# Kernel optimization log

Hardware: AMD Instinct MI355X
Metric: run time of the kernel (lower is better)

Reference implementation:

```python
import jax, jax.numpy as jnp
import numpy as np
from jax import lax

B, N, D = 4, 64, 32  # graphs, nodes/graph, volume side
HC = 1024            # hidden_channels
NF = 2048            # num_node_features = 32*(D//8)**3
NC = 4               # num_classes
LC = 256             # linear_channels = N*(HC//4)//64


def setup_inputs() -> dict:
    key = jax.random.key(0)
    ks = jax.random.split(key, 16)
    x = jax.random.normal(ks[0], (B, N, D, D, D), jnp.float32)
    # binary symmetric adjacency, zero diagonal (edge presence only; GCNConv ignores values)
    u = jax.random.uniform(ks[1], (B, N, N))
    a = (u < 0.2).astype(jnp.int32)
    a = jnp.maximum(a, a.transpose(0, 2, 1)) * (1 - jnp.eye(N, dtype=jnp.int32))
    s = 0.05
    inp = dict(
        x=x, adj=a, batch_size=B,
        w_conv1=jax.random.normal(ks[2], (16, 1, 3, 3, 3), jnp.float32) * s,
        b_conv1=jnp.zeros((16,), jnp.float32),
        w_conv2=jax.random.normal(ks[3], (32, 16, 3, 3, 3), jnp.float32) * s,
        b_conv2=jnp.zeros((32,), jnp.float32),
        w_g1=jax.random.normal(ks[4], (NF, HC), jnp.float32) * s,
        b_g1=jnp.zeros((HC,), jnp.float32),
        w_g2=jax.random.normal(ks[5], (HC, HC // 2), jnp.float32) * s,
        b_g2=jnp.zeros((HC // 2,), jnp.float32),
        w_g3=jax.random.normal(ks[6], (HC // 2, HC // 4), jnp.float32) * s,
        b_g3=jnp.zeros((HC // 4,), jnp.float32),
        w_fc1=jax.random.normal(ks[7], (LC, 2 * LC), jnp.float32) * s,
        b_fc1=jnp.zeros((2 * LC,), jnp.float32),
        w_fc2=jax.random.normal(ks[8], (2 * LC, NC), jnp.float32) * s,
        b_fc2=jnp.zeros((NC,), jnp.float32),
    )
    return inp


DN = ('NCDHW', 'OIDHW', 'NCDHW')


def _maxpool3(h):
    # MaxPool3d(kernel=3, stride=2, padding=1); pad value -inf matches torch
    return lax.reduce_window(h, -jnp.inf, lax.max,
                             (1, 1, 3, 3, 3), (1, 1, 2, 2, 2),
                             [(0, 0), (0, 0), (1, 1), (1, 1), (1, 1)])


def _gcn_norm(adj, dtype):
    # GCNConv: A_hat = A + I, sym-normalized D^-1/2 A_hat D^-1/2 (per graph)
    A = (adj != 0).astype(dtype) + jnp.eye(adj.shape[-1], dtype=dtype)[None]
    deg = A.sum(-1)                        # [B, N], >= 1
    dinv = deg ** -0.5
    return A * dinv[:, :, None] * dinv[:, None, :]


def _forward(x, adj, batch_size, w_conv1, b_conv1, w_conv2, b_conv2,
             w_g1, b_g1, w_g2, b_g2, w_g3, b_g3, w_fc1, b_fc1, w_fc2, b_fc2):
    b, n = x.shape[0], x.shape[1]
    v = x.reshape(b * n, 1, x.shape[2], x.shape[3], x.shape[4])
    h = lax.conv_general_dilated(v, w_conv1, (1, 1, 1), [(1, 1)] * 3, dimension_numbers=DN)
    h = jax.nn.relu(h + b_conv1[None, :, None, None, None])
    h = _maxpool3(h)                                     # [BN,16,16,16,16]
    h = lax.conv_general_dilated(h, w_conv2, (2, 2, 2), [(1, 1)] * 3, dimension_numbers=DN)
    h = jax.nn.relu(h + b_conv2[None, :, None, None, None])
    h = _maxpool3(h)                                     # [BN,32,4,4,4]
    feat = h.reshape(b, n, -1)                           # [B,N,2048]

    A_norm = _gcn_norm(adj, feat.dtype)                  # [B,N,N]
    gcn = lambda X, W, bb: jnp.einsum('bij,bjf->bif', A_norm, X @ W) + bb
    g = jax.nn.relu(gcn(feat, w_g1, b_g1))
    g = jax.nn.relu(gcn(g, w_g2, b_g2))
    g = gcn(g, w_g3, b_g3)                               # [B,N,256] (no relu, matches source)

    g = g.reshape(batch_size, -1)                        # [B, 16384]
    g = g.reshape(batch_size, -1, 64).max(-1)            # MaxPool1d(64) on 2D input -> [B,256]
    g = jax.nn.relu(g @ w_fc1 + b_fc1)
    return jax.nn.softmax(g @ w_fc2 + b_fc2, axis=-1)


def reference(x, adj, batch_size, w_conv1, b_conv1, w_conv2, b_conv2,
              w_g1, b_g1, w_g2, b_g2, w_g3, b_g3, w_fc1, b_fc1, w_fc2, b_fc2):
    return _forward(x, adj, batch_size, w_conv1, b_conv1, w_conv2, b_conv2,
                    w_g1, b_g1, w_g2, b_g2, w_g3, b_g3, w_fc1, b_fc1, w_fc2, b_fc2)
```

## Files before the change

### kernel.cpp

```cpp
#include <hip/hip_runtime.h>

typedef unsigned short ushort_t;
typedef unsigned long long ull_t;
typedef __attribute__((ext_vector_type(8))) short bf16x8;
typedef __attribute__((ext_vector_type(4))) float f32x4;

static __device__ __forceinline__ unsigned short f2bf(float f) {
  unsigned u = __float_as_uint(f);
  u = (u + 0x7FFFu + ((u >> 16) & 1u)) >> 16;
  return (unsigned short)u;
}

static __device__ __forceinline__ f32x4 max4(f32x4 a, f32x4 b) {
  f32x4 r;
  r[0] = fmaxf(a[0], b[0]); r[1] = fmaxf(a[1], b[1]);
  r[2] = fmaxf(a[2], b[2]); r[3] = fmaxf(a[3], b[3]);
  return r;
}

static __device__ __forceinline__ void gbar(int* bar0, int bid, bool do_wait) {
  __syncthreads();
  if (threadIdx.x == 0) {
    int* bar = bar0 + (bid << 10);
    __threadfence();
    const int leaf = (blockIdx.x & 7) << 5;
    if (__hip_atomic_fetch_add(&bar[leaf], 1, __ATOMIC_ACQ_REL,
                               __HIP_MEMORY_SCOPE_AGENT) == 7) {
      if (__hip_atomic_fetch_add(&bar[256], 1, __ATOMIC_ACQ_REL,
                                 __HIP_MEMORY_SCOPE_AGENT) == 7) {
#pragma unroll
        for (int i = 0; i < 8; ++i)
          __hip_atomic_store(&bar[288 + (i << 5)], 1, __ATOMIC_RELEASE,
                             __HIP_MEMORY_SCOPE_AGENT);
      }
    }
    if (do_wait) {
      int* mygen = &bar[288 + leaf];
      for (int it = 0; it < (1 << 22); ++it) {
        if (__hip_atomic_load(mygen, __ATOMIC_RELAXED,
                              __HIP_MEMORY_SCOPE_AGENT) != 0) break;
        __builtin_amdgcn_s_sleep(2);
      }
      __threadfence();
    }
  }
  __syncthreads();
}


__device__ __forceinline__ void prep_transpose(
    const float* __restrict__ W, ushort_t* __restrict__ out,
    int K, int N, int n0, int k0, int t, float (*tile)[33])
{
  const int tx = t & 31, ty = t >> 5;
#pragma unroll
  for (int i = 0; i < 4; ++i) {
    const int k = k0 + ty + i * 8;
    tile[ty + i * 8][tx] = W[(size_t)k * N + n0 + tx];
  }
  __syncthreads();
#pragma unroll
  for (int i = 0; i < 4; ++i) {
    const int n = n0 + ty + i * 8;
    out[(size_t)n * K + k0 + tx] = f2bf(tile[tx][ty + i * 8]);
  }
}

__global__ __launch_bounds__(256) void k_prep(
    const float* __restrict__ x, ushort_t* __restrict__ xb16,
    const float* __restrict__ w2, ushort_t* __restrict__ w2f,
    const float* __restrict__ wg1, ushort_t* __restrict__ wg1T,
    const float* __restrict__ wg2, ushort_t* __restrict__ wg2T,
    const float* __restrict__ wg3, ushort_t* __restrict__ wg3T,
    const int* __restrict__ adj, float* __restrict__ An)
{
  __shared__ float tile[32][33];
  __shared__ float dinv[64];
  __shared__ int part[256];
  int b = blockIdx.x;
  const int t = threadIdx.x;
  if (b < 8192) {
    const int tid = b * 256 + t;
    const float4 v = ((const float4*)x)[tid];
    const unsigned lo = (unsigned)f2bf(v.x) | ((unsigned)f2bf(v.y) << 16);
    const unsigned hi = (unsigned)f2bf(v.z) | ((unsigned)f2bf(v.w) << 16);
    ((uint2*)xb16)[tid] = make_uint2(lo, hi);
    return;
  }
  b -= 8192;
  if (b < 56) {
    const int tid = b * 256 + t;
    if (tid < 14336) {
      const int nt = tid / 7168, rem = tid % 7168;
      const int kk = rem / 512, rem2 = rem % 512;
      const int l = rem2 >> 3, j = rem2 & 7;
      const int n = nt * 16 + (l & 15);
      const int k = (l >> 4) * 8 + kk * 32 + j;
      float v = 0.f;
      if (k < 432) v = w2[n * 432 + k];
      w2f[tid] = f2bf(v);
    }
    return;
  }
  b -= 56;
  if (b < 2048) { prep_transpose(wg1, wg1T, 2048, 1024, (b & 31) << 5, (b >> 5) << 5, t, tile); return; }
  b -= 2048;
  if (b < 512)  { prep_transpose(wg2, wg2T, 1024, 512,  (b & 15) << 5, (b >> 4) << 5, t, tile); return; }
  b -= 512;
  if (b < 128)  { prep_transpose(wg3, wg3T, 512,  256,  (b & 7)  << 5, (b >> 3) << 5, t, tile); return; }
  b -= 128;
  {
    const int i = t >> 2, q = t & 3;
    const int* ab = adj + b * 4096 + i * 64 + q * 16;
    int d = 0;
#pragma unroll
    for (int j = 0; j < 16; ++j) d += (ab[j] != 0) ? 1 : 0;
    part[t] = d;
    __syncthreads();
    if (q == 0)
      dinv[i] = rsqrtf((float)(1 + part[t] + part[t + 1] + part[t + 2] + part[t + 3]));
    __syncthreads();
    for (int idx = t; idx < 4096; idx += 256) {
      const int ii = idx >> 6, jj = idx & 63;
      const float a = (ii == jj) ? 1.f : ((adj[b * 4096 + idx] != 0) ? 1.f : 0.f);
      An[b * 4096 + idx] = a * dinv[ii] * dinv[jj];
    }
  }
}

__global__ __launch_bounds__(256) void k_conv1_mfma(
    const ushort_t* __restrict__ xb16, const float* __restrict__ wc,
    const float* __restrict__ bc, ushort_t* __restrict__ h1)
{
  __shared__ ushort_t L[2 * 34 * 76];
  char* Lb = (char*)L;
  const int bn = blockIdx.x >> 3, zg = blockIdx.x & 7;
  const int t = threadIdx.x;
  const int w = t >> 6, l = t & 63;
  const int grp = l >> 4, m = l & 15, ch = l & 15;
  const float NINF = -1e30f;

  union { short s[8]; bf16x8 v; } uA, uB;
#pragma unroll
  for (int j = 0; j < 8; ++j) {
    const int k = grp * 8 + j;
    float wA = 0.f, wB = 0.f;
    if (k < 12) {
      const int dx = k >> 2, dz = k & 3;
      if (dz < 3) { wA = wc[ch*27 + dz*9 + 0 + dx]; wB = wc[ch*27 + dz*9 + 6 + dx]; }
    } else if (k >= 16 && k < 28) {
      const int kk = k - 16, dx = kk >> 2, dz = kk & 3;
      if (dz < 3) wA = wc[ch*27 + dz*9 + 3 + dx];
    }
    uA.s[j] = (short)f2bf(wA);
    uB.s[j] = (short)f2bf(wB);
  }

  int aX1[3], aX2[3];
#pragma unroll
  for (int s = 0; s < 3; ++s) {
    const int Q1 = 2*m + s + 2*(grp & 1);
    const int Q2 = Q1 + 1;
    aX1[s] = (Q1 & 1) * 5168 + (Q1 >> 1) * 8;
    aX2[s] = (Q2 & 1) * 5168 + (Q2 >> 1) * 8;
  }
  const int rsel = (grp >> 1) * 152;

  for (int u = t; u < 200; u += 256) {
    int addr;
    if (u < 72) {
      const int rr = (u < 36) ? 0 : 33;
      const int s = (u < 36) ? u : u - 36;
      const int pp = s / 18, slot = s - pp * 18;
      addr = pp * 5168 + rr * 152 + slot * 8;
    } else {
      const int v = u - 72;
      const int rr = 1 + (v >> 2);
      const int pp = (v >> 1) & 1;
      const int slot = (v & 1) * 17;
      addr = pp * 5168 + rr * 152 + slot * 8;
    }
    *(ull_t*)(Lb + addr) = 0ull;
  }

  f32x4 accZ[4][2];
#pragma unroll
  for (int j = 0; j < 4; ++j)
#pragma unroll
    for (int p = 0; p < 2; ++p) accZ[j][p] = (f32x4){NINF, NINF, NINF, NINF};

  const ushort_t* xb = xb16 + (size_t)bn * 32768;

#pragma unroll 1
  for (int ci = 0; ci < 5; ++ci) {
    const int cz = 4*zg - 1 + ci;
    if (cz < 0) continue;
    if (t < 128) {
      const int r = 1 + (t >> 2), g = t & 3;
      const ushort_t* xrow = xb + (r - 1) * 32 + g * 8;
      uint4 u0 = make_uint4(0u, 0u, 0u, 0u), u2 = make_uint4(0u, 0u, 0u, 0u);
      if (cz > 0)  u0 = *(const uint4*)(xrow + (cz - 1) * 1024);
      const uint4 u1 = *(const uint4*)(xrow + cz * 1024);
      if (cz < 31) u2 = *(const uint4*)(xrow + (cz + 1) * 1024);
      char* b0 = Lb + r * 152 + (4 * g + 1) * 8;
      char* b1 = Lb + 5168 + r * 152 + (4 * g + 1) * 8;
      const unsigned* p0 = (const unsigned*)&u0;
      const unsigned* p1 = (const unsigned*)&u1;
      const unsigned* p2 = (const unsigned*)&u2;
#pragma unroll
      for (int e = 0; e < 4; ++e) {
        const unsigned w0 = p0[e], w1 = p1[e], w2v = p2[e];
        const unsigned lo_e = (w0 & 0xFFFFu) | (w1 << 16);
        const unsigned hi_e = (w2v & 0xFFFFu);
        const unsigned lo_o = (w0 >> 16) | (w1 & 0xFFFF0000u);
        const unsigned hi_o = (w2v >> 16);
        *(ull_t*)(b0 + e * 8) = (ull_t)lo_e | ((ull_t)hi_e << 32);
        *(ull_t*)(b1 + e * 8) = (ull_t)lo_o | ((ull_t)hi_o << 32);
      }
    }
    __syncthreads();
    f32x4 accP0 = (f32x4){NINF, NINF, NINF, NINF};
    f32x4 accP1 = (f32x4){NINF, NINF, NINF, NINF};
#pragma unroll
    for (int yy = 0; yy < 9; ++yy) {
      if (yy == 0 && w == 0) continue;
      const int y = 8 * w - 1 + yy;
      const int rbA = y * 152 + rsel;
      const int rbB = (y + 2) * 152;
      f32x4 Cy;
#pragma unroll
      for (int s = 0; s < 3; ++s) {
        union { ull_t u[2]; bf16x8 v; } fA, fB;
        fA.u[0] = *(const ull_t*)(Lb + aX1[s] + rbA);
        fA.u[1] = *(const ull_t*)(Lb + aX2[s] + rbA);
        fB.u[0] = *(const ull_t*)(Lb + aX1[s] + rbB);
        fB.u[1] = *(const ull_t*)(Lb + aX2[s] + rbB);
        f32x4 acc = (f32x4){0.f, 0.f, 0.f, 0.f};
        acc = __builtin_amdgcn_mfma_f32_16x16x32_bf16(fA.v, uA.v, acc, 0, 0, 0);
        acc = __builtin_amdgcn_mfma_f32_16x16x32_bf16(fB.v, uB.v, acc, 0, 0, 0);
        if (s == 0) acc[0] = (l < 16) ? NINF : acc[0];
        Cy = (s == 0) ? acc : max4(Cy, acc);
      }
      if (yy & 1) {
        const int c = (yy - 1) / 2;
        if ((c & 1) == 0) accP0 = max4(accP0, Cy); else accP1 = max4(accP1, Cy);
      } else {
        const int cl = yy / 2 - 1;
        const int chh = yy / 2;
        if (cl >= 0) {
          if ((cl & 1) == 0) {
            accP0 = max4(accP0, Cy);
            if (ci <= 2) accZ[cl][0] = max4(accZ[cl][0], accP0);
            if (ci >= 2) accZ[cl][1] = max4(accZ[cl][1], accP0);
            accP0 = (f32x4){NINF, NINF, NINF, NINF};
          } else {
            accP1 = max4(accP1, Cy);
            if (ci <= 2) accZ[cl][0] = max4(accZ[cl][0], accP1);
            if (ci >= 2) accZ[cl][1] = max4(accZ[cl][1], accP1);
            accP1 = (f32x4){NINF, NINF, NINF, NINF};
          }
        }
        if (chh <= 3) {
          if ((chh & 1) == 0) accP0 = max4(accP0, Cy); else accP1 = max4(accP1, Cy);
        }
      }
    }
    __syncthreads();
  }

  const float biasv = bc[ch];
#pragma unroll
  for (int j = 0; j < 4; ++j) {
    const int py = 4 * w + j;
#pragma unroll
    for (int p = 0; p < 2; ++p) {
      const int pz = 2 * zg + p;
      const f32x4 v = accZ[j][p];
      const unsigned lo = (unsigned)f2bf(fmaxf(v[0] + biasv, 0.f)) |
                          ((unsigned)f2bf(fmaxf(v[1] + biasv, 0.f)) << 16);
      const unsigned hi = (unsigned)f2bf(fmaxf(v[2] + biasv, 0.f)) |
                          ((unsigned)f2bf(fmaxf(v[3] + biasv, 0.f)) << 16);
      ushort_t* dst = h1 + (((size_t)(bn * 16 + ch) * 16 + pz) << 8) + py * 16 + grp * 4;
      *(uint2*)dst = make_uint2(lo, hi);
    }
  }
}

__global__ __launch_bounds__(128) void k_conv2(
    const ushort_t* __restrict__ h1, const ushort_t* __restrict__ w2f,
    float* __restrict__ c2)
{
  __shared__ ushort_t U[16 * 456];
  ushort_t* Hs = U;
  unsigned* Hsd = (unsigned*)U;
  ushort_t* As = U;
  const int b = blockIdx.x;
  const int bn = b >> 5, oz = (b >> 2) & 7, yg = b & 3;
  const int t = threadIdx.x;
  const ushort_t* hb = h1 + ((size_t)bn << 16);
  const int w = t >> 6, l = t & 63;

  bf16x8 bfr[14];
#pragma unroll
  for (int kk = 0; kk < 14; ++kk)
    bfr[kk] = *(const bf16x8*)(const void*)&w2f[(((w * 14) + kk) * 64 + l) * 8];

#pragma unroll
  for (int it = 0; it < 9; ++it) {
    const int u = t + it * 128;
    const int row = u >> 2, q = u & 3;
    const int ic = row / 18;
    const int r2 = row - ic * 18;
    const int izp = r2 / 6;
    const int iyp = r2 - izp * 6;
    const int iz = 2 * oz - 1 + izp;
    const int iy = 4 * yg - 1 + iyp;
    uint2 v = make_uint2(0u, 0u);
    if ((unsigned)iz < 16u && (unsigned)iy < 16u)
      v = *(const uint2*)(hb + (ic << 12) + (iz << 8) + (iy << 4) + q * 4);
    *(uint2*)&Hs[row * 20 + q * 4] = v;
  }
  __syncthreads();

  const int m = t >> 3, sub = t & 7;
  const int ox = m & 7;
  const int my = (m >> 3) * 2;
  ushort_t tv[54];
  int j = 0;
#pragma unroll
  for (int ic2 = 0; ic2 < 2; ++ic2) {
    const int ic = sub * 2 + ic2;
#pragma unroll
    for (int dz = 0; dz < 3; ++dz) {
#pragma unroll
      for (int dy = 0; dy < 3; ++dy) {
        const int row = ic * 18 + dz * 6 + my + dy;
        const unsigned* rp = Hsd + row * 10;
        const unsigned d0 = (ox > 0) ? rp[ox - 1] : 0u;
        const unsigned d1 = rp[ox];
        tv[j]     = (ushort_t)(d0 >> 16);
        tv[j + 1] = (ushort_t)(d1 & 0xFFFFu);
        tv[j + 2] = (ushort_t)(d1 >> 16);
        j += 3;
      }
    }
  }
  __syncthreads();

  {
    unsigned* Aw = (unsigned*)As;
    const int wbase = m * 228 + sub * 27;
#pragma unroll
    for (int p = 0; p < 27; ++p)
      Aw[wbase + p] = (unsigned)tv[2 * p] | ((unsigned)tv[2 * p + 1] << 16);
    Aw[(t >> 3) * 228 + 216 + (t & 7)] = 0u;
  }
  __syncthreads();

  f32x4 acc = {0.f, 0.f, 0.f, 0.f};
  const ushort_t* arow = &As[(l & 15) * 456 + ((l >> 4) << 3)];
#pragma unroll
  for (int kk = 0; kk < 14; ++kk) {
    const bf16x8 af = *(const bf16x8*)(const void*)&arow[kk * 32];
    acc = __builtin_amdgcn_mfma_f32_16x16x32_bf16(af, bfr[kk], acc, 0, 0, 0);
  }
  const int n = w * 16 + (l & 15);
  const int m0 = (l >> 4) << 2;
  float* cb = c2 + (((size_t)(bn * 32 + n) * 8) + oz) * 64 + yg * 16 + m0;
  *(float4*)cb = make_float4(acc[0], acc[1], acc[2], acc[3]);
}

__global__ __launch_bounds__(256) void k_pool2(
    const float* __restrict__ c2, const float* __restrict__ bc2,
    ushort_t* __restrict__ featb, int* __restrict__ bar)
{
  if (blockIdx.x == 0) {
    for (int i = threadIdx.x; i < 4096; i += 256) bar[i] = 0;
  }
  const int tid = blockIdx.x * 256 + threadIdx.x;
  const int bn = tid >> 9, r = tid & 511;
  const int ch = r >> 4, pz = (r >> 2) & 3, py = r & 3;
  const float* base = c2 + ((size_t)(bn * 32 + ch) << 9);
  float m0 = -1e30f, m1 = -1e30f, m2 = -1e30f, m3 = -1e30f;
#pragma unroll
  for (int dz = 0; dz < 3; ++dz) {
    const int oz = 2 * pz - 1 + dz;
    if ((unsigned)oz >= 8u) continue;
#pragma unroll
    for (int dy = 0; dy < 3; ++dy) {
      const int oy = 2 * py - 1 + dy;
      if ((unsigned)oy >= 8u) continue;
      const float* row = base + (oz << 6) + (oy << 3);
      const float4 a = ((const float4*)row)[0];
      const float4 b = ((const float4*)row)[1];
      m0 = fmaxf(m0, fmaxf(a.x, a.y));
      m1 = fmaxf(m1, fmaxf(a.y, fmaxf(a.z, a.w)));
      m2 = fmaxf(m2, fmaxf(a.w, fmaxf(b.x, b.y)));
      m3 = fmaxf(m3, fmaxf(b.y, fmaxf(b.z, b.w)));
    }
  }
  const float bb = bc2[ch];
  const unsigned lo = (unsigned)f2bf(fmaxf(m0 + bb, 0.f)) |
                      ((unsigned)f2bf(fmaxf(m1 + bb, 0.f)) << 16);
  const unsigned hi = (unsigned)f2bf(fmaxf(m2 + bb, 0.f)) |
                      ((unsigned)f2bf(fmaxf(m3 + bb, 0.f)) << 16);
  *(uint2*)(featb + (size_t)bn * 2048 + r * 4) = make_uint2(lo, hi);
}

__device__ __forceinline__ void gcn_body(
    const ushort_t* __restrict__ Xb, const ushort_t* __restrict__ WT,
    const float* __restrict__ bias, const float* __restrict__ An,
    ushort_t* __restrict__ Ob, float* __restrict__ spw,
    int K, int N, int relu, int b, int jb,
    ushort_t (*As)[64 * 72], ushort_t (*Bs)[64 * 72], ushort_t* Ps)
{
  const int t = threadIdx.x, w = t >> 6, l = t & 63;
  const int r0 = t >> 3, kc0 = t & 7;
  const int lm = l & 15, lg = l >> 4;

  union { short s[8]; bf16x8 v; } afr[2];
  {
    const float* ap = An + b * 4096 + (16 * w + lm) * 64 + (lg << 3);
#pragma unroll
    for (int kc = 0; kc < 2; ++kc) {
      const float4 v0 = *(const float4*)(ap + kc * 32);
      const float4 v1 = *(const float4*)(ap + kc * 32 + 4);
      afr[kc].s[0] = (short)f2bf(v0.x); afr[kc].s[1] = (short)f2bf(v0.y);
      afr[kc].s[2] = (short)f2bf(v0.z); afr[kc].s[3] = (short)f2bf(v0.w);
      afr[kc].s[4] = (short)f2bf(v1.x); afr[kc].s[5] = (short)f2bf(v1.y);
      afr[kc].s[6] = (short)f2bf(v1.z); afr[kc].s[7] = (short)f2bf(v1.w);
    }
  }

  f32x4 acc[4];
#pragma unroll
  for (int nt = 0; nt < 4; ++nt) acc[nt] = (f32x4){0.f, 0.f, 0.f, 0.f};

  const ushort_t* arow0 = &Xb[(size_t)(b * 64 + r0) * K + kc0 * 8];
  const ushort_t* arow1 = &Xb[(size_t)(b * 64 + r0 + 32) * K + kc0 * 8];
  const ushort_t* brow0 = &WT[(size_t)(jb + r0) * K + kc0 * 8];
  const ushort_t* brow1 = &WT[(size_t)(jb + r0 + 32) * K + kc0 * 8];

  uint4 vaA0 = *(const uint4*)arow0;
  uint4 vaA1 = *(const uint4*)arow1;
  uint4 vbA0 = *(const uint4*)brow0;
  uint4 vbA1 = *(const uint4*)brow1;
  uint4 vaB0 = *(const uint4*)(arow0 + 64);
  uint4 vaB1 = *(const uint4*)(arow1 + 64);
  uint4 vbB0 = *(const uint4*)(brow0 + 64);
  uint4 vbB1 = *(const uint4*)(brow1 + 64);

  int buf = 0;
#pragma unroll 1
  for (int kt = 0; kt < K; kt += 128) {
    *(uint4*)&As[buf][r0 * 72 + kc0 * 8]        = vaA0;
    *(uint4*)&As[buf][(r0 + 32) * 72 + kc0 * 8] = vaA1;
    *(uint4*)&Bs[buf][r0 * 72 + kc0 * 8]        = vbA0;
    *(uint4*)&Bs[buf][(r0 + 32) * 72 + kc0 * 8] = vbA1;
    __syncthreads();
    if (kt + 128 < K) {
      vaA0 = *(const uint4*)(arow0 + kt + 128);
      vaA1 = *(const uint4*)(arow1 + kt + 128);
      vbA0 = *(const uint4*)(brow0 + kt + 128);
      vbA1 = *(const uint4*)(brow1 + kt + 128);
    }
#pragma unroll
    for (int ks = 0; ks < 2; ++ks) {
      const bf16x8 af = *(const bf16x8*)(const void*)
          &As[buf][(16 * w + lm) * 72 + ks * 32 + (lg << 3)];
#pragma unroll
      for (int nt = 0; nt < 4; ++nt) {
        const bf16x8 bf = *(const bf16x8*)(const void*)
            &Bs[buf][(nt * 16 + lm) * 72 + ks * 32 + (lg << 3)];
        acc[nt] = __builtin_amdgcn_mfma_f32_16x16x32_bf16(af, bf, acc[nt], 0, 0, 0);
      }
    }
    buf ^= 1;
    *(uint4*)&As[buf][r0 * 72 + kc0 * 8]        = vaB0;
    *(uint4*)&As[buf][(r0 + 32) * 72 + kc0 * 8] = vaB1;
    *(uint4*)&Bs[buf][r0 * 72 + kc0 * 8]        = vbB0;
    *(uint4*)&Bs[buf][(r0 + 32) * 72 + kc0 * 8] = vbB1;
    __syncthreads();
    if (kt + 192 < K) {
      vaB0 = *(const uint4*)(arow0 + kt + 192);
      vaB1 = *(const uint4*)(arow1 + kt + 192);
      vbB0 = *(const uint4*)(brow0 + kt + 192);
      vbB1 = *(const uint4*)(brow1 + kt + 192);
    }
#pragma unroll
    for (int ks = 0; ks < 2; ++ks) {
      const bf16x8 af = *(const bf16x8*)(const void*)
          &As[buf][(16 * w + lm) * 72 + ks * 32 + (lg << 3)];
#pragma unroll
      for (int nt = 0; nt < 4; ++nt) {
        const bf16x8 bf = *(const bf16x8*)(const void*)
            &Bs[buf][(nt * 16 + lm) * 72 + ks * 32 + (lg << 3)];
        acc[nt] = __builtin_amdgcn_mfma_f32_16x16x32_bf16(af, bf, acc[nt], 0, 0, 0);
      }
    }
    buf ^= 1;
  }

  __syncthreads();
  const int m0 = lg << 2;
#pragma unroll
  for (int nt = 0; nt < 4; ++nt) {
    const int n = nt * 16 + lm;
    const unsigned lo = (unsigned)f2bf(acc[nt][0]) | ((unsigned)f2bf(acc[nt][1]) << 16);
    const unsigned hi = (unsigned)f2bf(acc[nt][2]) | ((unsigned)f2bf(acc[nt][3]) << 16);
    *(uint2*)&Ps[n * 72 + 16 * w + m0] = make_uint2(lo, hi);
  }
  __syncthreads();

  float mx0 = -1e30f, mx1 = -1e30f, mx2 = -1e30f, mx3 = -1e30f;
#pragma unroll
  for (int nt = 0; nt < 4; ++nt) {
    const bf16x8 b0 = *(const bf16x8*)(const void*)&Ps[(nt * 16 + lm) * 72 + (lg << 3)];
    const bf16x8 b1 = *(const bf16x8*)(const void*)&Ps[(nt * 16 + lm) * 72 + 32 + (lg << 3)];
    f32x4 a2 = (f32x4){0.f, 0.f, 0.f, 0.f};
    a2 = __builtin_amdgcn_mfma_f32_16x16x32_bf16(afr[0].v, b0, a2, 0, 0, 0);
    a2 = __builtin_amdgcn_mfma_f32_16x16x32_bf16(afr[1].v, b1, a2, 0, 0, 0);
    const int col = jb + nt * 16 + lm;
    const float bv = bias[col];
    if (spw) {
      mx0 = fmaxf(mx0, a2[0] + bv);
      mx1 = fmaxf(mx1, a2[1] + bv);
      mx2 = fmaxf(mx2, a2[2] + bv);
      mx3 = fmaxf(mx3, a2[3] + bv);
    } else {
#pragma unroll
      for (int r = 0; r < 4; ++r) {
        const int row = b * 64 + 16 * w + m0 + r;
        float v = a2[r] + bv;
        if (relu) v = fmaxf(v, 0.f);
        Ob[(size_t)row * N + col] = f2bf(v);
      }
    }
  }
  if (spw) {
#pragma unroll
    for (int mk = 1; mk <= 8; mk <<= 1) {
      mx0 = fmaxf(mx0, __shfl_xor(mx0, mk));
      mx1 = fmaxf(mx1, __shfl_xor(mx1, mk));
      mx2 = fmaxf(mx2, __shfl_xor(mx2, mk));
      mx3 = fmaxf(mx3, __shfl_xor(mx3, mk));
    }
    if (lm == 0) {
      const int c = jb >> 6;
      const int n = 16 * w + m0;
      spw[b * 256 + (n + 0) * 4 + c] = mx0;
      spw[b * 256 + (n + 1) * 4 + c] = mx1;
      spw[b * 256 + (n + 2) * 4 + c] = mx2;
      spw[b * 256 + (n + 3) * 4 + c] = mx3;
    }
  }
}

__global__ __launch_bounds__(256) void k_tail(
    const ushort_t* __restrict__ featb,
    const ushort_t* __restrict__ wg1T, const float* __restrict__ bg1,
    const ushort_t* __restrict__ wg2T, const float* __restrict__ bg2,
    const ushort_t* __restrict__ wg3T, const float* __restrict__ bg3,
    const float* __restrict__ An,
    ushort_t* __restrict__ g1b, ushort_t* __restrict__ g2b,
    float* __restrict__ spw, float* __restrict__ shw,
    const float* __restrict__ w1, const float* __restrict__ b1,
    const float* __restrict__ w2, const float* __restrict__ b2,
    float* __restrict__ out, int* __restrict__ bar)
{
  __shared__ ushort_t As[2][64 * 72];
  __shared__ ushort_t Bs[2][64 * 72];
  __shared__ ushort_t Ps[64 * 72];
  __shared__ float red[260];
  const int bx = blockIdx.x, t = threadIdx.x;

  gcn_body(featb, wg1T, bg1, An, g1b, nullptr, 2048, 1024, 1,
           bx >> 4, (bx & 15) << 6, As, Bs, Ps);
  gbar(bar, 0, bx < 32);

  if (bx < 32)
    gcn_body(g1b, wg2T, bg2, An, g2b, nullptr, 1024, 512, 1,
             bx >> 3, (bx & 7) << 6, As, Bs, Ps);
  gbar(bar, 1, bx < 16);

  if (bx < 16)
    gcn_body(g2b, wg3T, bg3, An, nullptr, spw, 512, 256, 0,
             bx >> 2, (bx & 3) << 6, As, Bs, Ps);
  gbar(bar, 2, true);

  {
    const int oo = t & 31, ks = t >> 5;
    const int bb = bx >> 4;
    const int jj = (bx & 15) * 32 + oo;
    const float* spb = spw + bb * 256;
    float s = 0.f;
#pragma unroll
    for (int i = 0; i < 32; ++i) {
      const int k = ks * 32 + i;
      s += spb[k] * w1[k * 512 + jj];
    }
    red[t] = s;
    __syncthreads();
    if (t < 32) {
      float s2 = 0.f;
#pragma unroll
      for (int i = 0; i < 8; ++i) s2 += red[t + i * 32];
      const int j2 = (bx & 15) * 32 + t;
      shw[bb * 512 + j2] = fmaxf(s2 + b1[j2], 0.f);
    }
  }
  gbar(bar, 3, bx < 4);

  if (bx < 4) {
    float s = 0.f;
    if (t < 128) {
      const int c = t & 3, ks2 = t >> 2;
      const float* shb = shw + bx * 512;
#pragma unroll
      for (int i = 0; i < 16; ++i) {
        const int k = ks2 * 16 + i;
        s += shb[k] * w2[k * 4 + c];
      }
    }
    red[t] = s;
    __syncthreads();
    if (t < 4) {
      float s2 = b2[t];
#pragma unroll
      for (int i = 0; i < 32; ++i) s2 += red[t + i * 4];
      red[256 + t] = s2;
    }
    __syncthreads();
    if (t == 0) {
      const float a0 = red[256], a1 = red[257], a2v = red[258], a3 = red[259];
      const float mm = fmaxf(fmaxf(a0, a1), fmaxf(a2v, a3));
      const float e0 = expf(a0 - mm), e1 = expf(a1 - mm);
      const float e2 = expf(a2v - mm), e3 = expf(a3 - mm);
      const float inv = 1.f / (e0 + e1 + e2 + e3);
      out[bx * 4 + 0] = e0 * inv;
      out[bx * 4 + 1] = e1 * inv;
      out[bx * 4 + 2] = e2 * inv;
      out[bx * 4 + 3] = e3 * inv;
    }
  }
}

extern "C" void kernel_launch(void* const* d_in, const int* in_sizes, int n_in,
                              void* d_out, int out_size, void* d_ws, size_t ws_size,
                              hipStream_t stream)
{
  (void)in_sizes; (void)n_in; (void)out_size; (void)ws_size;
  const float* x   = (const float*)d_in[0];
  const int*   adj = (const int*)d_in[1];
  const float* wc1 = (const float*)d_in[3];
  const float* bc1 = (const float*)d_in[4];
  const float* wc2 = (const float*)d_in[5];
  const float* bc2 = (const float*)d_in[6];
  const float* wg1 = (const float*)d_in[7];
  const float* bg1 = (const float*)d_in[8];
  const float* wg2 = (const float*)d_in[9];
  const float* bg2 = (const float*)d_in[10];
  const float* wg3 = (const float*)d_in[11];
  const float* bg3 = (const float*)d_in[12];
  const float* wf1 = (const float*)d_in[13];
  const float* bf1 = (const float*)d_in[14];
  const float* wf2 = (const float*)d_in[15];
  const float* bf2 = (const float*)d_in[16];

  float* ws    = (float*)d_ws;
  ushort_t* h1 = (ushort_t*)d_ws;
  ushort_t* w2f   = (ushort_t*)(ws + 8388608);
  ushort_t* wg1Tb = (ushort_t*)(ws + 8395776);
  ushort_t* wg2Tb = (ushort_t*)(ws + 9444352);
  ushort_t* wg3Tb = (ushort_t*)(ws + 9706496);
  ushort_t* featb = (ushort_t*)(ws + 9772032);
  ushort_t* g1b   = (ushort_t*)(ws + 10034176);
  ushort_t* g2b   = (ushort_t*)(ws + 10165248);
  float* c2    = ws + 16777216;
  ushort_t* xb16 = (ushort_t*)(ws + 16777216);
  float* An   = ws + 21495808;
  float* spw  = ws + 2621440;
  float* shw  = ws + 2622464;
  int*   bar  = (int*)(ws + 22364160);
  float* outp = (float*)d_out;

  hipLaunchKernelGGL(k_prep,        dim3(10940),    dim3(256), 0, stream,
                     x, xb16, wc2, w2f, wg1, wg1Tb, wg2, wg2Tb, wg3, wg3Tb, adj, An);
  hipLaunchKernelGGL(k_conv1_mfma,  dim3(2048),     dim3(256), 0, stream, xb16, wc1, bc1, h1);
  hipLaunchKernelGGL(k_conv2,       dim3(8192),     dim3(128), 0, stream, h1, w2f, c2);
  hipLaunchKernelGGL(k_pool2,       dim3(512),      dim3(256), 0, stream, c2, bc2, featb, bar);
  hipLaunchKernelGGL(k_tail,        dim3(64),       dim3(256), 0, stream,
                     featb, wg1Tb, bg1, wg2Tb, bg2, wg3Tb, bg3, An, g1b, g2b,
                     spw, shw, wf1, bf1, wf2, bf2, outp, bar);
}
```

Measured before the change: 249.0 us.

## Fuse conv2 max-pool into tail kernel and store conv2 output as bf16

Conv2 now writes its pre-bias output as packed bf16 instead of fp32, which halves the intermediate traffic. The separate pool kernel is removed, and the pool stage now runs as the first phase of an enlarged 512-block tail kernel. A grid barrier sits between the pool phase and the GCN phases, and the extra blocks exit after it. The goal is to save one kernel launch and some memory traffic. In exchange, every tail kernel launch pays for a 512-block grid barrier, and rounding the pre-pool values to bf16 adds a small precision loss. The grid barrier also depends on all 512 blocks being resident at the same time.

```diff
diff --git a/kernel.cpp b/kernel.cpp
--- a/kernel.cpp
+++ b/kernel.cpp
@@ -18,14 +18,16 @@
   return r;
 }
 
-static __device__ __forceinline__ void gbar(int* bar0, int bid, bool do_wait) {
+static __device__ __forceinline__ void gbar(int* bar0, int bid, int nb,
+                                            bool do_wait) {
   __syncthreads();
   if (threadIdx.x == 0) {
     int* bar = bar0 + (bid << 10);
     __threadfence();
     const int leaf = (blockIdx.x & 7) << 5;
+    const int nleaf = nb >> 3;
     if (__hip_atomic_fetch_add(&bar[leaf], 1, __ATOMIC_ACQ_REL,
-                               __HIP_MEMORY_SCOPE_AGENT) == 7) {
+                               __HIP_MEMORY_SCOPE_AGENT) == nleaf - 1) {
       if (__hip_atomic_fetch_add(&bar[256], 1, __ATOMIC_ACQ_REL,
                                  __HIP_MEMORY_SCOPE_AGENT) == 7) {
 #pragma unroll
@@ -288,7 +290,7 @@
 
 __global__ __launch_bounds__(128) void k_conv2(
     const ushort_t* __restrict__ h1, const ushort_t* __restrict__ w2f,
-    float* __restrict__ c2)
+    ushort_t* __restrict__ c2b, int* __restrict__ bar)
 {
   __shared__ ushort_t U[16 * 456];
   ushort_t* Hs = U;
@@ -299,6 +301,10 @@
   const int t = threadIdx.x;
   const ushort_t* hb = h1 + ((size_t)bn << 16);
   const int w = t >> 6, l = t & 63;
+
+  if (b == 0) {
+    for (int i = t; i < 5120; i += 128) bar[i] = 0;
+  }
 
   bf16x8 bfr[14];
 #pragma unroll
@@ -366,45 +372,10 @@
   }
   const int n = w * 16 + (l & 15);
   const int m0 = (l >> 4) << 2;
-  float* cb = c2 + (((size_t)(bn * 32 + n) * 8) + oz) * 64 + yg * 16 + m0;
-  *(float4*)cb = make_float4(acc[0], acc[1], acc[2], acc[3]);
-}
-
-__global__ __launch_bounds__(256) void k_pool2(
-    const float* __restrict__ c2, const float* __restrict__ bc2,
-    ushort_t* __restrict__ featb, int* __restrict__ bar)
-{
-  if (blockIdx.x == 0) {
-    for (int i = threadIdx.x; i < 4096; i += 256) bar[i] = 0;
-  }
-  const int tid = blockIdx.x * 256 + threadIdx.x;
-  const int bn = tid >> 9, r = tid & 511;
-  const int ch = r >> 4, pz = (r >> 2) & 3, py = r & 3;
-  const float* base = c2 + ((size_t)(bn * 32 + ch) << 9);
-  float m0 = -1e30f, m1 = -1e30f, m2 = -1e30f, m3 = -1e30f;
-#pragma unroll
-  for (int dz = 0; dz < 3; ++dz) {
-    const int oz = 2 * pz - 1 + dz;
-    if ((unsigned)oz >= 8u) continue;
-#pragma unroll
-    for (int dy = 0; dy < 3; ++dy) {
-      const int oy = 2 * py - 1 + dy;
-      if ((unsigned)oy >= 8u) continue;
-      const float* row = base + (oz << 6) + (oy << 3);
-      const float4 a = ((const float4*)row)[0];
-      const float4 b = ((const float4*)row)[1];
-      m0 = fmaxf(m0, fmaxf(a.x, a.y));
-      m1 = fmaxf(m1, fmaxf(a.y, fmaxf(a.z, a.w)));
-      m2 = fmaxf(m2, fmaxf(a.w, fmaxf(b.x, b.y)));
-      m3 = fmaxf(m3, fmaxf(b.y, fmaxf(b.z, b.w)));
-    }
-  }
-  const float bb = bc2[ch];
-  const unsigned lo = (unsigned)f2bf(fmaxf(m0 + bb, 0.f)) |
-                      ((unsigned)f2bf(fmaxf(m1 + bb, 0.f)) << 16);
-  const unsigned hi = (unsigned)f2bf(fmaxf(m2 + bb, 0.f)) |
-                      ((unsigned)f2bf(fmaxf(m3 + bb, 0.f)) << 16);
-  *(uint2*)(featb + (size_t)bn * 2048 + r * 4) = make_uint2(lo, hi);
+  ushort_t* cb = c2b + (((size_t)(bn * 32 + n) * 8) + oz) * 64 + yg * 16 + m0;
+  const unsigned lo = (unsigned)f2bf(acc[0]) | ((unsigned)f2bf(acc[1]) << 16);
+  const unsigned hi = (unsigned)f2bf(acc[2]) | ((unsigned)f2bf(acc[3]) << 16);
+  *(uint2*)cb = make_uint2(lo, hi);
 }
 
 __device__ __forceinline__ void gcn_body(
@@ -557,7 +528,8 @@
 }
 
 __global__ __launch_bounds__(256) void k_tail(
-    const ushort_t* __restrict__ featb,
+    const ushort_t* __restrict__ c2b, const float* __restrict__ bc2,
+    ushort_t* __restrict__ featb,
     const ushort_t* __restrict__ wg1T, const float* __restrict__ bg1,
     const ushort_t* __restrict__ wg2T, const float* __restrict__ bg2,
     const ushort_t* __restrict__ wg3T, const float* __restrict__ bg3,
@@ -574,19 +546,58 @@
   __shared__ float red[260];
   const int bx = blockIdx.x, t = threadIdx.x;
 
+  {
+    const int tid = bx * 256 + t;
+    const int bn = tid >> 9, r = tid & 511;
+    const int ch = r >> 4, pz = (r >> 2) & 3, py = r & 3;
+    const ushort_t* base = c2b + ((size_t)(bn * 32 + ch) << 9);
+    float m0 = -1e30f, m1 = -1e30f, m2 = -1e30f, m3 = -1e30f;
+#pragma unroll
+    for (int dz = 0; dz < 3; ++dz) {
+      const int oz = 2 * pz - 1 + dz;
+      if ((unsigned)oz >= 8u) continue;
+#pragma unroll
+      for (int dy = 0; dy < 3; ++dy) {
+        const int oy = 2 * py - 1 + dy;
+        if ((unsigned)oy >= 8u) continue;
+        const uint4 v = *(const uint4*)(base + (oz << 6) + (oy << 3));
+        const float x0 = __uint_as_float((v.x & 0xFFFFu) << 16);
+        const float x1 = __uint_as_float(v.x & 0xFFFF0000u);
+        const float x2 = __uint_as_float((v.y & 0xFFFFu) << 16);
+        const float x3 = __uint_as_float(v.y & 0xFFFF0000u);
+        const float x4 = __uint_as_float((v.z & 0xFFFFu) << 16);
+        const float x5 = __uint_as_float(v.z & 0xFFFF0000u);
+        const float x6 = __uint_as_float((v.w & 0xFFFFu) << 16);
+        const float x7 = __uint_as_float(v.w & 0xFFFF0000u);
+        m0 = fmaxf(m0, fmaxf(x0, x1));
+        m1 = fmaxf(m1, fmaxf(x1, fmaxf(x2, x3)));
+        m2 = fmaxf(m2, fmaxf(x3, fmaxf(x4, x5)));
+        m3 = fmaxf(m3, fmaxf(x5, fmaxf(x6, x7)));
+      }
+    }
+    const float bb = bc2[ch];
+    const unsigned lo = (unsigned)f2bf(fmaxf(m0 + bb, 0.f)) |
+                        ((unsigned)f2bf(fmaxf(m1 + bb, 0.f)) << 16);
+    const unsigned hi = (unsigned)f2bf(fmaxf(m2 + bb, 0.f)) |
+                        ((unsigned)f2bf(fmaxf(m3 + bb, 0.f)) << 16);
+    *(uint2*)(featb + (size_t)bn * 2048 + r * 4) = make_uint2(lo, hi);
+  }
+  gbar(bar, 0, 512, bx < 64);
+  if (bx >= 64) return;
+
   gcn_body(featb, wg1T, bg1, An, g1b, nullptr, 2048, 1024, 1,
            bx >> 4, (bx & 15) << 6, As, Bs, Ps);
-  gbar(bar, 0, bx < 32);
+  gbar(bar, 1, 64, bx < 32);
 
   if (bx < 32)
     gcn_body(g1b, wg2T, bg2, An, g2b, nullptr, 1024, 512, 1,
              bx >> 3, (bx & 7) << 6, As, Bs, Ps);
-  gbar(bar, 1, bx < 16);
+  gbar(bar, 2, 64, bx < 16);
 
   if (bx < 16)
     gcn_body(g2b, wg3T, bg3, An, nullptr, spw, 512, 256, 0,
              bx >> 2, (bx & 3) << 6, As, Bs, Ps);
-  gbar(bar, 2, true);
+  gbar(bar, 3, 64, true);
 
   {
     const int oo = t & 31, ks = t >> 5;
@@ -609,7 +620,7 @@
       shw[bb * 512 + j2] = fmaxf(s2 + b1[j2], 0.f);
     }
   }
-  gbar(bar, 3, bx < 4);
+  gbar(bar, 4, 64, bx < 4);
 
   if (bx < 4) {
     float s = 0.f;
@@ -676,7 +687,7 @@
   ushort_t* featb = (ushort_t*)(ws + 9772032);
   ushort_t* g1b   = (ushort_t*)(ws + 10034176);
   ushort_t* g2b   = (ushort_t*)(ws + 10165248);
-  float* c2    = ws + 16777216;
+  ushort_t* c2b  = (ushort_t*)(ws + 16777216);
   ushort_t* xb16 = (ushort_t*)(ws + 16777216);
   float* An   = ws + 21495808;
   float* spw  = ws + 2621440;
@@ -687,9 +698,8 @@
   hipLaunchKernelGGL(k_prep,        dim3(10940),    dim3(256), 0, stream,
                      x, xb16, wc2, w2f, wg1, wg1Tb, wg2, wg2Tb, wg3, wg3Tb, adj, An);
   hipLaunchKernelGGL(k_conv1_mfma,  dim3(2048),     dim3(256), 0, stream, xb16, wc1, bc1, h1);
-  hipLaunchKernelGGL(k_conv2,       dim3(8192),     dim3(128), 0, stream, h1, w2f, c2);
-  hipLaunchKernelGGL(k_pool2,       dim3(512),      dim3(256), 0, stream, c2, bc2, featb, bar);
-  hipLaunchKernelGGL(k_tail,        dim3(64),       dim3(256), 0, stream,
-                     featb, wg1Tb, bg1, wg2Tb, bg2, wg3Tb, bg3, An, g1b, g2b,
-                     spw, shw, wf1, bf1, wf2, bf2, outp, bar);
-}
+  hipLaunchKernelGGL(k_conv2,       dim3(8192),     dim3(128), 0, stream, h1, w2f, c2b, bar);
+  hipLaunchKernelGGL(k_tail,        dim3(512),      dim3(256), 0, stream,
+                     c2b, bc2, featb, wg1Tb, bg1, wg2Tb, bg2, wg3Tb, bg3, An,
+                     g1b, g2b, spw, shw, wf1, bf1, wf2, bf2, outp, bar);
+}
```

New measurement: 272.8 us. +9.5%, slower.
